# Performance work log

Measured on AMD Instinct MI355X. Metric: run time of the kernel, lower is better.

The kernel has to match this reference:

```python
import jax, jax.numpy as jnp
import numpy as np

N, BSZ, NE, DIN, DH, RH = 32, 512, 7, 512, 256, 64
NPAIR = NE * (NE - 1) // 2  # 21
PAIRS = [(i, j) for i in range(NE) for j in range(i + 1, NE)]


def setup_inputs() -> dict:
    key = jax.random.key(0)
    ks = jax.random.split(key, 16)
    def w(k, shape, fan_in):
        return jax.random.normal(k, shape, jnp.float32) / np.sqrt(fan_in)
    return {
        "input": jax.random.normal(ks[0], (N, BSZ, NE, DIN), jnp.float32),
        "ctx_differences": jax.random.normal(ks[1], (BSZ, NPAIR, 5), jnp.float32),
        "lang_input": jax.random.normal(ks[2], (N, BSZ, 128), jnp.float32),
        "num_markables": jax.random.randint(ks[3], (BSZ,), 0, N),
        # unary feedforward: 2 hidden layers + output layer (output_dim=2)
        "W0": w(ks[4], (DIN, DH), DIN), "b0": jnp.zeros((DH,), jnp.float32),
        "W1": w(ks[5], (DH, DH), DH), "b1": jnp.zeros((DH,), jnp.float32),
        "W2": w(ks[6], (DH, 2), DH), "b2": jnp.zeros((2,), jnp.float32),
        # relation encoder: 1 hidden layer (dim 64), output 3
        "R0": w(ks[7], (5, RH), 5), "r0": jnp.zeros((RH,), jnp.float32),
        "R1": w(ks[8], (RH, 3), RH), "r1": jnp.zeros((3,), jnp.float32),
    }


def reference(input, ctx_differences, lang_input, num_markables,
              W0, b0, W1, b1, W2, b2, R0, r0, R1, r1):
    # unary potentials: [N, bsz, 7, 2]
    h = jax.nn.relu(input @ W0 + b0)
    h = jax.nn.relu(h @ W1 + b1)
    un = h @ W2 + b2
    # binary potentials: [bsz, 21, 3] -> map to 2x2 via fixed matrix
    h2 = jax.nn.relu(ctx_differences @ R0 + r0)
    bp3 = h2 @ R1 + r1
    Mmap = jnp.array([[1, 0, 0], [0, 1, 0], [0, 1, 0], [0, 0, 1]], jnp.float32)
    bp4 = jnp.einsum('bpx,yx->bpy', bp3, Mmap).reshape(BSZ, NPAIR, 2, 2)

    # accumulate log-factors into the joint log tensor [N, bsz, 2,...,2]
    joint = jnp.zeros((N, BSZ) + (2,) * NE, jnp.float32)
    for i in range(NE):
        shp = [N, BSZ] + [1] * NE
        shp[2 + i] = 2
        joint = joint + un[:, :, i].reshape(shp)
    for p, (i, j) in enumerate(PAIRS):
        shp = [1, BSZ] + [1] * NE
        shp[2 + i] = 2
        shp[2 + j] = 2
        joint = joint + bp4[:, p].reshape(shp)

    # marginals: logsumexp over all entity axes but one -> [N, bsz, 7, 2]
    ent_axes = tuple(range(2, 2 + NE))
    marg = jnp.stack(
        [jax.scipy.special.logsumexp(joint, axis=tuple(a for a in ent_axes if a != 2 + i))
         for i in range(NE)], axis=2)
    lm = jax.nn.log_softmax(marg, axis=-1)
    marginal_log_probs = lm[..., 1] - lm[..., 0]  # [N, bsz, 7]

    jf = joint.reshape(N, BSZ, 2 ** NE)
    joint_log_probs = jax.nn.log_softmax(jf, axis=-1).reshape((N, BSZ) + (2,) * NE)
    return (marginal_log_probs, joint_log_probs)
```

## Files before the change

### kernel.cpp

```cpp
#include <hip/hip_runtime.h>

typedef __bf16 bf16;
typedef bf16 bf16x8 __attribute__((ext_vector_type(8)));
typedef bf16 bf16x4 __attribute__((ext_vector_type(4)));
typedef float f32x4 __attribute__((ext_vector_type(4)));

#define MFMA(a, b, c) __builtin_amdgcn_mfma_f32_16x16x32_bf16((a), (b), (c), 0, 0, 0)


__global__ __launch_bounds__(256) void k_prep(const float* __restrict__ W0,
                                              const float* __restrict__ W1,
                                              const float* __restrict__ W2,
                                              bf16* __restrict__ W0f,
                                              bf16* __restrict__ W1f,
                                              bf16* __restrict__ W2f) {
  int g = blockIdx.x * 256 + threadIdx.x;
  if (g < 16384) {
    int mt = g >> 10, ks = (g >> 6) & 15, lane = g & 63;
    int m = mt * 16 + (lane & 15);
    int kb = ks * 32 + (lane >> 4) * 8;
    bf16x8 v;
#pragma unroll
    for (int j = 0; j < 8; ++j) v[j] = (bf16)W0[(kb + j) * 256 + m];
    *(bf16x8*)&W0f[g * 8] = v;
  } else if (g < 24576) {
    int h = g - 16384;
    int mt = h >> 9, ks = (h >> 6) & 7, lane = h & 63;
    int m = mt * 16 + (lane & 15);
    int kb = ks * 32 + (lane >> 4) * 8;
    bf16x8 v;
#pragma unroll
    for (int j = 0; j < 8; ++j) v[j] = (bf16)W1[(kb + j) * 256 + m];
    *(bf16x8*)&W1f[h * 8] = v;
  } else {
    int h = g - 24576;
    int ks = h >> 6, lane = h & 63;
    int c = lane & 15;
    int kb = ks * 32 + (lane >> 4) * 8;
    bf16x8 v;
#pragma unroll
    for (int j = 0; j < 8; ++j) v[j] = (c < 2) ? (bf16)W2[(kb + j) * 2 + c] : (bf16)0.0f;
    *(bf16x8*)&W2f[h * 8] = v;
  }
}

__global__ __launch_bounds__(256, 2) void k_unary(const float* __restrict__ input,
                                                  const bf16* __restrict__ W0f,
                                                  const bf16* __restrict__ W1f,
                                                  const bf16* __restrict__ W2f,
                                                  const float* __restrict__ b0,
                                                  const float* __restrict__ b1,
                                                  const float* __restrict__ b2,
                                                  float* __restrict__ un) {
  __shared__ bf16 inp_lds[64 * 40];
  __shared__ bf16 h_lds[64 * 264];
  __shared__ float bias_lds[512];
  __shared__ float part_lds[512];

  const int tid = threadIdx.x;
  const int wave = tid >> 6;
  const int lane = tid & 63;
  const int l16 = lane & 15;
  const int lq = lane >> 4;
  const long m0 = (long)blockIdx.x * 64;

  bias_lds[tid] = b0[tid];
  bias_lds[256 + tid] = b1[tid];

  f32x4 acc[4][4];
#pragma unroll
  for (int i = 0; i < 4; ++i)
#pragma unroll
    for (int j = 0; j < 4; ++j) acc[i][j] = (f32x4){0.f, 0.f, 0.f, 0.f};

  const int r = tid >> 2;
  const int q = tid & 3;
  const float* gp = input + (m0 + r) * 512 + q * 8;
  float4 xa = *(const float4*)gp;
  float4 xb = *(const float4*)(gp + 4);

  for (int it = 0; it < 16; ++it) {
    __syncthreads();
    bf16x8 w;
    w[0] = (bf16)xa.x; w[1] = (bf16)xa.y; w[2] = (bf16)xa.z; w[3] = (bf16)xa.w;
    w[4] = (bf16)xb.x; w[5] = (bf16)xb.y; w[6] = (bf16)xb.z; w[7] = (bf16)xb.w;
    *(bf16x8*)&inp_lds[r * 40 + q * 8] = w;
    __syncthreads();
    if (it < 15) {
      gp += 32;
      xa = *(const float4*)gp;
      xb = *(const float4*)(gp + 4);
    }
    bf16x8 bfr[4];
#pragma unroll
    for (int nt = 0; nt < 4; ++nt)
      bfr[nt] = *(const bf16x8*)&inp_lds[(nt * 16 + l16) * 40 + lq * 8];
#pragma unroll
    for (int mt = 0; mt < 4; ++mt) {
      bf16x8 a = *(const bf16x8*)&W0f[(((wave * 4 + mt) * 16 + it) * 64 + lane) * 8];
#pragma unroll
      for (int nt = 0; nt < 4; ++nt) acc[mt][nt] = MFMA(a, bfr[nt], acc[mt][nt]);
    }
  }

#pragma unroll
  for (int mt = 0; mt < 4; ++mt) {
    const int nbase = (wave * 4 + mt) * 16 + lq * 4;
    float bb[4];
#pragma unroll
    for (int g = 0; g < 4; ++g) bb[g] = bias_lds[nbase + g];
#pragma unroll
    for (int nt = 0; nt < 4; ++nt) {
      const int m = nt * 16 + l16;
      bf16x4 hv;
#pragma unroll
      for (int g = 0; g < 4; ++g) hv[g] = (bf16)fmaxf(acc[mt][nt][g] + bb[g], 0.f);
      *(bf16x4*)&h_lds[m * 264 + nbase] = hv;
    }
  }
  __syncthreads();

#pragma unroll
  for (int i = 0; i < 4; ++i)
#pragma unroll
    for (int j = 0; j < 4; ++j) acc[i][j] = (f32x4){0.f, 0.f, 0.f, 0.f};
  for (int ks = 0; ks < 8; ++ks) {
    bf16x8 bfr[4];
#pragma unroll
    for (int nt = 0; nt < 4; ++nt)
      bfr[nt] = *(const bf16x8*)&h_lds[(nt * 16 + l16) * 264 + ks * 32 + lq * 8];
#pragma unroll
    for (int mt = 0; mt < 4; ++mt) {
      bf16x8 a = *(const bf16x8*)&W1f[(((wave * 4 + mt) * 8 + ks) * 64 + lane) * 8];
#pragma unroll
      for (int nt = 0; nt < 4; ++nt) acc[mt][nt] = MFMA(a, bfr[nt], acc[mt][nt]);
    }
  }
  __syncthreads();

#pragma unroll
  for (int mt = 0; mt < 4; ++mt) {
    const int nbase = (wave * 4 + mt) * 16 + lq * 4;
    float bb[4];
#pragma unroll
    for (int g = 0; g < 4; ++g) bb[g] = bias_lds[256 + nbase + g];
#pragma unroll
    for (int nt = 0; nt < 4; ++nt) {
      const int m = nt * 16 + l16;
      bf16x4 hv;
#pragma unroll
      for (int g = 0; g < 4; ++g) hv[g] = (bf16)fmaxf(acc[mt][nt][g] + bb[g], 0.f);
      *(bf16x4*)&h_lds[m * 264 + nbase] = hv;
    }
  }
  __syncthreads();

  f32x4 acc2[4];
#pragma unroll
  for (int i = 0; i < 4; ++i) acc2[i] = (f32x4){0.f, 0.f, 0.f, 0.f};
#pragma unroll
  for (int s = 0; s < 2; ++s) {
    const int ks = wave * 2 + s;
    bf16x8 a = *(const bf16x8*)&W2f[(ks * 64 + lane) * 8];
#pragma unroll
    for (int nt = 0; nt < 4; ++nt) {
      bf16x8 b = *(const bf16x8*)&h_lds[(nt * 16 + l16) * 264 + ks * 32 + lq * 8];
      acc2[nt] = MFMA(a, b, acc2[nt]);
    }
  }
  if (lane < 16) {
#pragma unroll
    for (int nt = 0; nt < 4; ++nt) {
      part_lds[((wave * 4 + nt) * 16 + lane) * 2 + 0] = acc2[nt][0];
      part_lds[((wave * 4 + nt) * 16 + lane) * 2 + 1] = acc2[nt][1];
    }
  }
  __syncthreads();
  if (tid < 128) {
    const int mloc = tid >> 1, c = tid & 1;
    const int nt = mloc >> 4, l = mloc & 15;
    float s = b2[c];
#pragma unroll
    for (int w2 = 0; w2 < 4; ++w2) s += part_lds[((w2 * 4 + nt) * 16 + l) * 2 + c];
    un[(m0 + mloc) * 2 + c] = s;
  }
}

__global__ __launch_bounds__(128) void k_bsum(const float* __restrict__ ctx,
                                              const float* __restrict__ R0,
                                              const float* __restrict__ r0,
                                              const float* __restrict__ R1,
                                              const float* __restrict__ r1,
                                              float* __restrict__ bsum) {
  __shared__ float ctx_l[105], R0_l[320], r0_l[64], R1_l[192], r1_l[3];
  __shared__ float h2[21 * 65];
  __shared__ float bp[63];
  const int t = threadIdx.x;
  const int b = blockIdx.x;
  if (t < 105) ctx_l[t] = ctx[b * 105 + t];
  for (int i = t; i < 320; i += 128) R0_l[i] = R0[i];
  if (t < 64) r0_l[t] = r0[t];
  for (int i = t; i < 192; i += 128) R1_l[i] = R1[i];
  if (t < 3) r1_l[t] = r1[t];
  __syncthreads();
  for (int idx = t; idx < 1344; idx += 128) {
    int p = idx >> 6, u = idx & 63;
    float a = r0_l[u];
#pragma unroll
    for (int x = 0; x < 5; ++x) a += ctx_l[p * 5 + x] * R0_l[x * 64 + u];
    h2[p * 65 + u] = fmaxf(a, 0.f);
  }
  __syncthreads();
  if (t < 63) {
    int p = t / 3, y = t - p * 3;
    float a = r1_l[y];
    for (int u = 0; u < 64; ++u) a += h2[p * 65 + u] * R1_l[u * 3 + y];
    bp[t] = a;
  }
  __syncthreads();
  float a = 0.f;
  int pi = 0;
#pragma unroll
  for (int i = 0; i < 7; ++i)
#pragma unroll
    for (int j = i + 1; j < 7; ++j) {
      int bi = (t >> (6 - i)) & 1, bj = (t >> (6 - j)) & 1;
      a += bp[pi * 3 + bi + bj];
      ++pi;
    }
  bsum[b * 128 + t] = a;
}

__global__ __launch_bounds__(128) void k_joint(const float* __restrict__ un,
                                               const float* __restrict__ bsum,
                                               float* __restrict__ out_marg,
                                               float* __restrict__ out_joint) {
  __shared__ float u_l[14];
  __shared__ float wred[16];
  const int t = threadIdx.x;
  const int blk = blockIdx.x;
  const int n = blk & 31, b = blk >> 5;
  const long row = (long)n * 512 + b;
  if (t < 14) u_l[t] = un[row * 14 + t];
  __syncthreads();
  float j = bsum[b * 128 + t];
#pragma unroll
  for (int i = 0; i < 7; ++i) j += u_l[i * 2 + ((t >> (6 - i)) & 1)];
  const int w = t >> 6, lane = t & 63;
  float m = j;
#pragma unroll
  for (int o = 32; o; o >>= 1) m = fmaxf(m, __shfl_xor(m, o, 64));
  if (lane == 0) wred[w * 8 + 7] = m;
  __syncthreads();
  m = fmaxf(wred[7], wred[15]);
  float e = __expf(j - m);
  float tot = e;
#pragma unroll
  for (int o = 32; o; o >>= 1) tot += __shfl_xor(tot, o, 64);
  float s1q[6];
#pragma unroll
  for (int qb = 0; qb < 6; ++qb) {
    float v = ((lane >> qb) & 1) ? e : 0.f;
#pragma unroll
    for (int o = 32; o; o >>= 1) v += __shfl_xor(v, o, 64);
    s1q[qb] = v;
  }
  if (lane == 0) {
    wred[w * 8 + 0] = tot;
#pragma unroll
    for (int qb = 0; qb < 6; ++qb) wred[w * 8 + 1 + qb] = s1q[qb];
  }
  __syncthreads();
  const float T = wred[0] + wred[8];
  const float lT = __logf(T);
  out_joint[row * 128 + t] = (j - m) - lT;
  if (t < 7) {
    float s1, s0;
    if (t == 0) { s1 = wred[8]; s0 = wred[0]; }
    else {
      const int qb = 6 - t;
      s1 = wred[1 + qb] + wred[8 + 1 + qb];
      s0 = T - s1;
    }
    out_marg[row * 7 + t] = __logf(s1) - __logf(s0);
  }
}

extern "C" void kernel_launch(void* const* d_in, const int* in_sizes, int n_in,
                              void* d_out, int out_size, void* d_ws, size_t ws_size,
                              hipStream_t stream) {
  const float* input = (const float*)d_in[0];
  const float* ctx   = (const float*)d_in[1];
  const float* W0 = (const float*)d_in[4];
  const float* b0 = (const float*)d_in[5];
  const float* W1 = (const float*)d_in[6];
  const float* b1 = (const float*)d_in[7];
  const float* W2 = (const float*)d_in[8];
  const float* b2 = (const float*)d_in[9];
  const float* R0 = (const float*)d_in[10];
  const float* r0 = (const float*)d_in[11];
  const float* R1 = (const float*)d_in[12];
  const float* r1 = (const float*)d_in[13];

  char* ws = (char*)d_ws;
  bf16* W0f  = (bf16*)(ws + 0);
  bf16* W1f  = (bf16*)(ws + 262144);
  bf16* W2f  = (bf16*)(ws + 393216);
  float* un  = (float*)(ws + 401408);
  float* bsm = (float*)(ws + 1318912);

  float* out_marg = (float*)d_out;
  float* out_joint = out_marg + 114688;

  hipLaunchKernelGGL(k_prep, dim3(98), dim3(256), 0, stream, W0, W1, W2, W0f, W1f, W2f);
  hipLaunchKernelGGL(k_bsum, dim3(512), dim3(128), 0, stream, ctx, R0, r0, R1, r1, bsm);
  hipLaunchKernelGGL(k_unary, dim3(1792), dim3(256), 0, stream,
                     input, W0f, W1f, W2f, b0, b1, b2, un);
  hipLaunchKernelGGL(k_joint, dim3(16384), dim3(128), 0, stream, un, bsm, out_marg, out_joint);
}
```

Before: 401.6 us.

## Fuse prep and bsum kernels, widen unary K-step, wave-per-row joint kernel

Merges the weight-repack and pair-potential kernels into one launch. In the unary GEMM it doubles the K chunk staged per LDS round, halving the number of barriers, raises the occupancy hint to 3 blocks, and unrolls the second GEMM loop. It also rewrites the joint/marginal kernel so each wave handles one (n,b) row entirely with shuffles and no LDS or barriers, packing four rows per block. The risks are register pressure from the higher occupancy target and the larger staging buffer.

```diff
diff --git a/kernel.cpp b/kernel.cpp
--- a/kernel.cpp
+++ b/kernel.cpp
@@ -8,43 +8,86 @@
 #define MFMA(a, b, c) __builtin_amdgcn_mfma_f32_16x16x32_bf16((a), (b), (c), 0, 0, 0)
 
 
-__global__ __launch_bounds__(256) void k_prep(const float* __restrict__ W0,
-                                              const float* __restrict__ W1,
-                                              const float* __restrict__ W2,
-                                              bf16* __restrict__ W0f,
-                                              bf16* __restrict__ W1f,
-                                              bf16* __restrict__ W2f) {
-  int g = blockIdx.x * 256 + threadIdx.x;
-  if (g < 16384) {
-    int mt = g >> 10, ks = (g >> 6) & 15, lane = g & 63;
-    int m = mt * 16 + (lane & 15);
-    int kb = ks * 32 + (lane >> 4) * 8;
-    bf16x8 v;
-#pragma unroll
-    for (int j = 0; j < 8; ++j) v[j] = (bf16)W0[(kb + j) * 256 + m];
-    *(bf16x8*)&W0f[g * 8] = v;
-  } else if (g < 24576) {
-    int h = g - 16384;
-    int mt = h >> 9, ks = (h >> 6) & 7, lane = h & 63;
-    int m = mt * 16 + (lane & 15);
-    int kb = ks * 32 + (lane >> 4) * 8;
-    bf16x8 v;
-#pragma unroll
-    for (int j = 0; j < 8; ++j) v[j] = (bf16)W1[(kb + j) * 256 + m];
-    *(bf16x8*)&W1f[h * 8] = v;
+__global__ __launch_bounds__(256) void k_prep_bsum(
+    const float* __restrict__ W0, const float* __restrict__ W1,
+    const float* __restrict__ W2, bf16* __restrict__ W0f,
+    bf16* __restrict__ W1f, bf16* __restrict__ W2f,
+    const float* __restrict__ ctx, const float* __restrict__ R0,
+    const float* __restrict__ r0, const float* __restrict__ R1,
+    const float* __restrict__ r1, float* __restrict__ bsum) {
+  if (blockIdx.x < 98) {
+    int g = blockIdx.x * 256 + threadIdx.x;
+    if (g < 16384) {
+      int mt = g >> 10, ks = (g >> 6) & 15, lane = g & 63;
+      int m = mt * 16 + (lane & 15);
+      int kb = ks * 32 + (lane >> 4) * 8;
+      bf16x8 v;
+#pragma unroll
+      for (int j = 0; j < 8; ++j) v[j] = (bf16)W0[(kb + j) * 256 + m];
+      *(bf16x8*)&W0f[g * 8] = v;
+    } else if (g < 24576) {
+      int h = g - 16384;
+      int mt = h >> 9, ks = (h >> 6) & 7, lane = h & 63;
+      int m = mt * 16 + (lane & 15);
+      int kb = ks * 32 + (lane >> 4) * 8;
+      bf16x8 v;
+#pragma unroll
+      for (int j = 0; j < 8; ++j) v[j] = (bf16)W1[(kb + j) * 256 + m];
+      *(bf16x8*)&W1f[h * 8] = v;
+    } else {
+      int h = g - 24576;
+      int ks = h >> 6, lane = h & 63;
+      int c = lane & 15;
+      int kb = ks * 32 + (lane >> 4) * 8;
+      bf16x8 v;
+#pragma unroll
+      for (int j = 0; j < 8; ++j) v[j] = (c < 2) ? (bf16)W2[(kb + j) * 2 + c] : (bf16)0.0f;
+      *(bf16x8*)&W2f[h * 8] = v;
+    }
   } else {
-    int h = g - 24576;
-    int ks = h >> 6, lane = h & 63;
-    int c = lane & 15;
-    int kb = ks * 32 + (lane >> 4) * 8;
-    bf16x8 v;
-#pragma unroll
-    for (int j = 0; j < 8; ++j) v[j] = (c < 2) ? (bf16)W2[(kb + j) * 2 + c] : (bf16)0.0f;
-    *(bf16x8*)&W2f[h * 8] = v;
+    __shared__ float ctx_l[105], R0_l[320], r0_l[64], R1_l[192], r1_l[3];
+    __shared__ float h2[21 * 65];
+    __shared__ float bp[63];
+    const int t = threadIdx.x;
+    const int b = blockIdx.x - 98;
+    if (t < 105) ctx_l[t] = ctx[b * 105 + t];
+    if (t < 64) r0_l[t] = r0[t];
+    if (t < 192) R1_l[t] = R1[t];
+    if (t < 3) r1_l[t] = r1[t];
+    for (int i = t; i < 320; i += 256) R0_l[i] = R0[i];
+    __syncthreads();
+    for (int idx = t; idx < 1344; idx += 256) {
+      int p = idx >> 6, u = idx & 63;
+      float a = r0_l[u];
+#pragma unroll
+      for (int x = 0; x < 5; ++x) a += ctx_l[p * 5 + x] * R0_l[x * 64 + u];
+      h2[p * 65 + u] = fmaxf(a, 0.f);
+    }
+    __syncthreads();
+    if (t < 63) {
+      int p = t / 3, y = t - p * 3;
+      float a = r1_l[y];
+      for (int u = 0; u < 64; ++u) a += h2[p * 65 + u] * R1_l[u * 3 + y];
+      bp[t] = a;
+    }
+    __syncthreads();
+    if (t < 128) {
+      float a = 0.f;
+      int pi = 0;
+#pragma unroll
+      for (int i = 0; i < 7; ++i)
+#pragma unroll
+        for (int j = i + 1; j < 7; ++j) {
+          int bi = (t >> (6 - i)) & 1, bj = (t >> (6 - j)) & 1;
+          a += bp[pi * 3 + bi + bj];
+          ++pi;
+        }
+      bsum[b * 128 + t] = a;
+    }
   }
 }
 
-__global__ __launch_bounds__(256, 2) void k_unary(const float* __restrict__ input,
+__global__ __launch_bounds__(256, 3) void k_unary(const float* __restrict__ input,
                                                   const bf16* __restrict__ W0f,
                                                   const bf16* __restrict__ W1f,
                                                   const bf16* __restrict__ W2f,
@@ -52,7 +95,7 @@
                                                   const float* __restrict__ b1,
                                                   const float* __restrict__ b2,
                                                   float* __restrict__ un) {
-  __shared__ bf16 inp_lds[64 * 40];
+  __shared__ bf16 inp_lds[64 * 68];
   __shared__ bf16 h_lds[64 * 264];
   __shared__ float bias_lds[512];
   __shared__ float part_lds[512];
@@ -75,31 +118,41 @@
 
   const int r = tid >> 2;
   const int q = tid & 3;
-  const float* gp = input + (m0 + r) * 512 + q * 8;
-  float4 xa = *(const float4*)gp;
-  float4 xb = *(const float4*)(gp + 4);
-
-  for (int it = 0; it < 16; ++it) {
-    __syncthreads();
-    bf16x8 w;
-    w[0] = (bf16)xa.x; w[1] = (bf16)xa.y; w[2] = (bf16)xa.z; w[3] = (bf16)xa.w;
-    w[4] = (bf16)xb.x; w[5] = (bf16)xb.y; w[6] = (bf16)xb.z; w[7] = (bf16)xb.w;
-    *(bf16x8*)&inp_lds[r * 40 + q * 8] = w;
-    __syncthreads();
-    if (it < 15) {
-      gp += 32;
-      xa = *(const float4*)gp;
-      xb = *(const float4*)(gp + 4);
-    }
-    bf16x8 bfr[4];
-#pragma unroll
-    for (int nt = 0; nt < 4; ++nt)
-      bfr[nt] = *(const bf16x8*)&inp_lds[(nt * 16 + l16) * 40 + lq * 8];
-#pragma unroll
-    for (int mt = 0; mt < 4; ++mt) {
-      bf16x8 a = *(const bf16x8*)&W0f[(((wave * 4 + mt) * 16 + it) * 64 + lane) * 8];
-#pragma unroll
-      for (int nt = 0; nt < 4; ++nt) acc[mt][nt] = MFMA(a, bfr[nt], acc[mt][nt]);
+  const float* gp = input + (m0 + r) * 512 + q * 16;
+  float4 x0 = ((const float4*)gp)[0];
+  float4 x1 = ((const float4*)gp)[1];
+  float4 x2 = ((const float4*)gp)[2];
+  float4 x3 = ((const float4*)gp)[3];
+
+  for (int it = 0; it < 8; ++it) {
+    __syncthreads();
+    bf16x8 wlo, whi;
+    wlo[0] = (bf16)x0.x; wlo[1] = (bf16)x0.y; wlo[2] = (bf16)x0.z; wlo[3] = (bf16)x0.w;
+    wlo[4] = (bf16)x1.x; wlo[5] = (bf16)x1.y; wlo[6] = (bf16)x1.z; wlo[7] = (bf16)x1.w;
+    whi[0] = (bf16)x2.x; whi[1] = (bf16)x2.y; whi[2] = (bf16)x2.z; whi[3] = (bf16)x2.w;
+    whi[4] = (bf16)x3.x; whi[5] = (bf16)x3.y; whi[6] = (bf16)x3.z; whi[7] = (bf16)x3.w;
+    *(bf16x8*)&inp_lds[r * 68 + q * 16] = wlo;
+    *(bf16x8*)&inp_lds[r * 68 + q * 16 + 8] = whi;
+    __syncthreads();
+    if (it < 7) {
+      gp += 64;
+      x0 = ((const float4*)gp)[0];
+      x1 = ((const float4*)gp)[1];
+      x2 = ((const float4*)gp)[2];
+      x3 = ((const float4*)gp)[3];
+    }
+#pragma unroll
+    for (int s = 0; s < 2; ++s) {
+      bf16x8 bfr[4];
+#pragma unroll
+      for (int nt = 0; nt < 4; ++nt)
+        bfr[nt] = *(const bf16x8*)&inp_lds[(nt * 16 + l16) * 68 + s * 32 + lq * 8];
+#pragma unroll
+      for (int mt = 0; mt < 4; ++mt) {
+        bf16x8 a = *(const bf16x8*)&W0f[(((wave * 4 + mt) * 16 + it * 2 + s) * 64 + lane) * 8];
+#pragma unroll
+        for (int nt = 0; nt < 4; ++nt) acc[mt][nt] = MFMA(a, bfr[nt], acc[mt][nt]);
+      }
     }
   }
 
@@ -124,6 +177,7 @@
   for (int i = 0; i < 4; ++i)
 #pragma unroll
     for (int j = 0; j < 4; ++j) acc[i][j] = (f32x4){0.f, 0.f, 0.f, 0.f};
+#pragma unroll
   for (int ks = 0; ks < 8; ++ks) {
     bf16x8 bfr[4];
 #pragma unroll
@@ -186,103 +240,48 @@
   }
 }
 
-__global__ __launch_bounds__(128) void k_bsum(const float* __restrict__ ctx,
-                                              const float* __restrict__ R0,
-                                              const float* __restrict__ r0,
-                                              const float* __restrict__ R1,
-                                              const float* __restrict__ r1,
-                                              float* __restrict__ bsum) {
-  __shared__ float ctx_l[105], R0_l[320], r0_l[64], R1_l[192], r1_l[3];
-  __shared__ float h2[21 * 65];
-  __shared__ float bp[63];
-  const int t = threadIdx.x;
-  const int b = blockIdx.x;
-  if (t < 105) ctx_l[t] = ctx[b * 105 + t];
-  for (int i = t; i < 320; i += 128) R0_l[i] = R0[i];
-  if (t < 64) r0_l[t] = r0[t];
-  for (int i = t; i < 192; i += 128) R1_l[i] = R1[i];
-  if (t < 3) r1_l[t] = r1[t];
-  __syncthreads();
-  for (int idx = t; idx < 1344; idx += 128) {
-    int p = idx >> 6, u = idx & 63;
-    float a = r0_l[u];
-#pragma unroll
-    for (int x = 0; x < 5; ++x) a += ctx_l[p * 5 + x] * R0_l[x * 64 + u];
-    h2[p * 65 + u] = fmaxf(a, 0.f);
-  }
-  __syncthreads();
-  if (t < 63) {
-    int p = t / 3, y = t - p * 3;
-    float a = r1_l[y];
-    for (int u = 0; u < 64; ++u) a += h2[p * 65 + u] * R1_l[u * 3 + y];
-    bp[t] = a;
-  }
-  __syncthreads();
-  float a = 0.f;
-  int pi = 0;
-#pragma unroll
-  for (int i = 0; i < 7; ++i)
-#pragma unroll
-    for (int j = i + 1; j < 7; ++j) {
-      int bi = (t >> (6 - i)) & 1, bj = (t >> (6 - j)) & 1;
-      a += bp[pi * 3 + bi + bj];
-      ++pi;
-    }
-  bsum[b * 128 + t] = a;
-}
-
-__global__ __launch_bounds__(128) void k_joint(const float* __restrict__ un,
+__global__ __launch_bounds__(256) void k_joint(const float* __restrict__ un,
                                                const float* __restrict__ bsum,
                                                float* __restrict__ out_marg,
                                                float* __restrict__ out_joint) {
-  __shared__ float u_l[14];
-  __shared__ float wred[16];
-  const int t = threadIdx.x;
-  const int blk = blockIdx.x;
-  const int n = blk & 31, b = blk >> 5;
-  const long row = (long)n * 512 + b;
-  if (t < 14) u_l[t] = un[row * 14 + t];
-  __syncthreads();
-  float j = bsum[b * 128 + t];
-#pragma unroll
-  for (int i = 0; i < 7; ++i) j += u_l[i * 2 + ((t >> (6 - i)) & 1)];
-  const int w = t >> 6, lane = t & 63;
-  float m = j;
-#pragma unroll
-  for (int o = 32; o; o >>= 1) m = fmaxf(m, __shfl_xor(m, o, 64));
-  if (lane == 0) wred[w * 8 + 7] = m;
-  __syncthreads();
-  m = fmaxf(wred[7], wred[15]);
-  float e = __expf(j - m);
-  float tot = e;
-#pragma unroll
-  for (int o = 32; o; o >>= 1) tot += __shfl_xor(tot, o, 64);
-  float s1q[6];
-#pragma unroll
-  for (int qb = 0; qb < 6; ++qb) {
-    float v = ((lane >> qb) & 1) ? e : 0.f;
-#pragma unroll
-    for (int o = 32; o; o >>= 1) v += __shfl_xor(v, o, 64);
-    s1q[qb] = v;
-  }
-  if (lane == 0) {
-    wred[w * 8 + 0] = tot;
-#pragma unroll
-    for (int qb = 0; qb < 6; ++qb) wred[w * 8 + 1 + qb] = s1q[qb];
-  }
-  __syncthreads();
-  const float T = wred[0] + wred[8];
-  const float lT = __logf(T);
-  out_joint[row * 128 + t] = (j - m) - lT;
-  if (t < 7) {
-    float s1, s0;
-    if (t == 0) { s1 = wred[8]; s0 = wred[0]; }
-    else {
-      const int qb = 6 - t;
-      s1 = wred[1 + qb] + wred[8 + 1 + qb];
-      s0 = T - s1;
-    }
-    out_marg[row * 7 + t] = __logf(s1) - __logf(s0);
+  const int lane = threadIdx.x & 63;
+  const int wave = threadIdx.x >> 6;
+  const int gw = blockIdx.x * 4 + wave;
+  const int b = gw & 511;
+  const long row = gw;
+  const int urow = __builtin_amdgcn_readfirstlane(gw);
+  float u[14];
+#pragma unroll
+  for (int i = 0; i < 14; ++i) u[i] = un[(long)urow * 14 + i];
+  const float bs0 = bsum[b * 128 + lane];
+  const float bs1 = bsum[b * 128 + 64 + lane];
+  float jc = 0.f;
+#pragma unroll
+  for (int i = 1; i < 7; ++i) jc += u[i * 2 + ((lane >> (6 - i)) & 1)];
+  const float j0 = bs0 + jc + u[0];
+  const float j1 = bs1 + jc + u[1];
+  float m = fmaxf(j0, j1);
+#pragma unroll
+  for (int o = 1; o < 64; o <<= 1) m = fmaxf(m, __shfl_xor(m, o, 64));
+  const float e0 = __expf(j0 - m), e1 = __expf(j1 - m);
+  float t = e0 + e1;
+  float s1e = e1;
+  float uu[6];
+#pragma unroll
+  for (int q = 0; q < 6; ++q) {
+    float pt = __shfl_xor(t, 1 << q, 64);
+    uu[q] = ((lane >> q) & 1) ? t : pt;
+    t += pt;
+    s1e += __shfl_xor(s1e, 1 << q, 64);
+#pragma unroll
+    for (int jq = 0; jq < q; ++jq) uu[jq] += __shfl_xor(uu[jq], 1 << q, 64);
+  }
+  const float lZ = m + __logf(t);
+  out_joint[row * 128 + lane] = j0 - lZ;
+  out_joint[row * 128 + 64 + lane] = j1 - lZ;
+  if (lane < 7) {
+    const float s1 = (lane == 0) ? s1e : uu[6 - lane];
+    out_marg[row * 7 + lane] = __logf(s1) - __logf(t - s1);
   }
 }
 
@@ -312,9 +311,9 @@
   float* out_marg = (float*)d_out;
   float* out_joint = out_marg + 114688;
 
-  hipLaunchKernelGGL(k_prep, dim3(98), dim3(256), 0, stream, W0, W1, W2, W0f, W1f, W2f);
-  hipLaunchKernelGGL(k_bsum, dim3(512), dim3(128), 0, stream, ctx, R0, r0, R1, r1, bsm);
+  hipLaunchKernelGGL(k_prep_bsum, dim3(610), dim3(256), 0, stream,
+                     W0, W1, W2, W0f, W1f, W2f, ctx, R0, r0, R1, r1, bsm);
   hipLaunchKernelGGL(k_unary, dim3(1792), dim3(256), 0, stream,
                      input, W0f, W1f, W2f, b0, b1, b2, un);
-  hipLaunchKernelGGL(k_joint, dim3(16384), dim3(128), 0, stream, un, bsm, out_marg, out_joint);
+  hipLaunchKernelGGL(k_joint, dim3(4096), dim3(256), 0, stream, un, bsm, out_marg, out_joint);
 }
```

New measurement: 409.4 us. About the same (+1.9%).
